# Kernel tuning notes

Hardware: AMD Instinct MI355X
Metric: run time of the kernel (lower is better)

The kernel has to match this reference:

```python
import jax, jax.numpy as jnp
import numpy as np

B, L, V = 64, 256, 8000
D_EMB = 100
D_MODEL = 256
H, DK = 4, 64
HID, HID2 = 256, 128   # bidirectional LSTM: 128 per direction
NT = 20                # tag_size
START, STOP = 18, 19


def setup_inputs() -> dict:
    key = jax.random.key(0)
    ks = jax.random.split(key, 32)
    s = 0.05
    inp = {}
    # forward args
    inp["sentences"] = jax.random.randint(ks[0], (B, L), 0, V)
    inp["bushou"] = jax.random.randint(ks[1], (B, L), 0, V)
    inp["pinyin"] = jax.random.normal(ks[2], (B, L, 20), dtype=jnp.float32)
    inp["weizhi"] = jax.random.normal(ks[3], (B, L, 18), dtype=jnp.float32)
    inp["trans_weizhi"] = jax.random.normal(ks[4], (B, L, 18), dtype=jnp.float32)
    inp["tags"] = jax.random.randint(ks[5], (B, L), 0, NT - 2)  # valid non-START/STOP tags
    inp["lengths"] = jax.random.randint(ks[6], (B,), L // 2, L + 1)
    # parameters
    inp["emb1"] = jax.random.normal(ks[7], (V, D_EMB)) * s
    inp["emb2"] = jax.random.normal(ks[8], (V, D_EMB)) * s
    inp["Wq"] = jax.random.normal(ks[9], (D_MODEL, D_MODEL)) * s
    inp["bq"] = jnp.zeros((D_MODEL,))
    inp["Wk"] = jax.random.normal(ks[10], (D_MODEL, D_MODEL)) * s
    inp["bk"] = jnp.zeros((D_MODEL,))
    inp["Wv"] = jax.random.normal(ks[11], (D_MODEL, D_MODEL)) * s
    inp["bv"] = jnp.zeros((D_MODEL,))
    inp["Wo"] = jax.random.normal(ks[12], (D_MODEL, D_MODEL)) * s
    inp["bo"] = jnp.zeros((D_MODEL,))
    # LSTM (torch layout): W_ih [4*HID2, D_MODEL], W_hh [4*HID2, HID2]; gate order i,f,g,o
    inp["Wih_f"] = jax.random.normal(ks[13], (4 * HID2, D_MODEL)) * s
    inp["Whh_f"] = jax.random.normal(ks[14], (4 * HID2, HID2)) * s
    inp["bih_f"] = jnp.zeros((4 * HID2,))
    inp["bhh_f"] = jnp.zeros((4 * HID2,))
    inp["Wih_b"] = jax.random.normal(ks[15], (4 * HID2, D_MODEL)) * s
    inp["Whh_b"] = jax.random.normal(ks[16], (4 * HID2, HID2)) * s
    inp["bih_b"] = jnp.zeros((4 * HID2,))
    inp["bhh_b"] = jnp.zeros((4 * HID2,))
    inp["Wout"] = jax.random.normal(ks[17], (NT, HID)) * s
    inp["bout"] = jnp.zeros((NT,))
    trans = jax.random.normal(ks[18], (NT, NT))
    trans = trans.at[:, START].set(-1000.0)
    trans = trans.at[STOP, :].set(-1000.0)
    inp["transitions"] = trans
    inp["h0"] = jax.random.normal(ks[19], (2, B, HID2))
    inp["c0"] = jax.random.normal(ks[20], (2, B, HID2))
    return inp


def _lstm_dir(x_tbd, Wih, Whh, bih, bhh, h0, c0, reverse):
    def step(carry, xt):
        h, c = carry
        g = xt @ Wih.T + bih + h @ Whh.T + bhh
        i, f, gg, o = jnp.split(g, 4, axis=-1)
        c = jax.nn.sigmoid(f) * c + jax.nn.sigmoid(i) * jnp.tanh(gg)
        h = jax.nn.sigmoid(o) * jnp.tanh(c)
        return (h, c), h
    _, ys = jax.lax.scan(step, (h0, c0), x_tbd, reverse=reverse)
    return ys  # [L, B, HID2], time-aligned


def reference(sentences, bushou, pinyin, weizhi, trans_weizhi, tags, lengths,
              emb1, emb2, Wq, bq, Wk, bk, Wv, bv, Wo, bo,
              Wih_f, Whh_f, bih_f, bhh_f, Wih_b, Whh_b, bih_b, bhh_b,
              Wout, bout, transitions, h0, c0):
    # feature concat: [emb1, emb2, pinyin, trans_weizhi, weizhi] -> [B,L,256]
    fin = jnp.concatenate([emb1[sentences], emb2[bushou], pinyin, trans_weizhi, weizhi], axis=2)

    def proj(W, b):
        return (fin @ W.T + b).reshape(B, L, H, DK).transpose(0, 2, 1, 3)  # [B,H,L,DK]
    q, k, v = proj(Wq, bq), proj(Wk, bk), proj(Wv, bv)
    scores = jnp.einsum('bhqd,bhkd->bhqk', q, k) / np.sqrt(DK).astype(np.float32)
    p = jax.nn.softmax(scores, axis=-1)  # dropout = identity at eval
    x = jnp.einsum('bhqk,bhkd->bhqd', p, v).transpose(0, 2, 1, 3).reshape(B, L, D_MODEL)
    x = x @ Wo.T + bo

    x_tbd = x.transpose(1, 0, 2)  # [L,B,256]
    out_f = _lstm_dir(x_tbd, Wih_f, Whh_f, bih_f, bhh_f, h0[0], c0[0], False)
    out_b = _lstm_dir(x_tbd, Wih_b, Whh_b, bih_b, bhh_b, h0[1], c0[1], True)
    lstm_out = jnp.concatenate([out_f, out_b], axis=-1).transpose(1, 0, 2)  # [B,L,256]
    logits = lstm_out @ Wout.T + bout  # [B,L,NT]

    mask = (jnp.arange(L)[None, :] < lengths[:, None])  # [B,L] valid positions

    # real path score (vectorized over batch, masked to length)
    lab = jnp.concatenate([jnp.full((B, 1), START, dtype=tags.dtype), tags], axis=1)  # [B,L+1]
    emis = jnp.take_along_axis(logits, tags[..., None], axis=2)[..., 0]  # [B,L]
    trans_step = transitions[lab[:, :-1], lab[:, 1:]]  # [B,L]
    last_tag = jnp.take_along_axis(tags, (lengths - 1)[:, None], axis=1)[:, 0]
    real = jnp.sum((emis + trans_step) * mask, axis=1) + transitions[last_tag, STOP]  # [B]

    # CRF forward algorithm (original initializes previous = zeros)
    def fstep(prev, inputs):
        logit_t, m_t = inputs  # [B,NT], [B]
        sc = prev[:, :, None] + transitions[None, :, :] + logit_t[:, None, :]  # [B,NT_prev,NT_cur]
        new = jax.nn.logsumexp(sc, axis=1)
        return jnp.where(m_t[:, None], new, prev), None
    prev0 = jnp.zeros((B, NT), dtype=logits.dtype)
    prev, _ = jax.lax.scan(fstep, prev0, (logits.transpose(1, 0, 2), mask.T))
    total = jax.nn.logsumexp(prev + transitions[:, STOP][None, :], axis=1)  # [B]

    return jnp.sum(total - real)  # neg log likelihood, summed over batch
```

## Files before the change

kernel.cpp:

```cpp
#include <hip/hip_runtime.h>
#include <math.h>

namespace {
constexpr int Bc = 64, Lc = 256, DMc = 256;
constexpr int NTc = 20, START_c = 18, STOP_c = 19;
constexpr int ROWSc = Bc * Lc;
}

typedef short short8 __attribute__((ext_vector_type(8)));
typedef float f32x4 __attribute__((ext_vector_type(4)));
typedef ushort ushort4v __attribute__((ext_vector_type(4)));
typedef unsigned int uint4v __attribute__((ext_vector_type(4)));

__device__ __forceinline__ ushort f2bf(float x) {
  unsigned u = __float_as_uint(x);
  unsigned r = (u + 0x7FFFu + ((u >> 16) & 1u)) >> 16;
  return (ushort)r;
}
__device__ __forceinline__ float bf2f(ushort h) {
  return __uint_as_float((unsigned)h << 16);
}
__device__ __forceinline__ float vrcp(float x) {
  float r;
  asm("v_rcp_f32 %0, %1" : "=v"(r) : "v"(x));
  return r;
}
__device__ __forceinline__ float fast_sig(float x) {
  return vrcp(1.f + __expf(-x));
}
__device__ __forceinline__ float fast_tanh(float x) {
  return fmaf(-2.f, vrcp(1.f + __expf(2.f * x)), 1.f);
}
__device__ __forceinline__ unsigned cvtpk(float a, float b) {
  unsigned r;
  asm("v_cvt_pk_bf16_f32 %0, %1, %2" : "=v"(r) : "v"(a), "v"(b));
  return r;
}

__global__ __launch_bounds__(256) void build_fin_k(
    const int* __restrict__ sent, const int* __restrict__ bush,
    const float* __restrict__ pin, const float* __restrict__ wz,
    const float* __restrict__ twz, const float* __restrict__ emb1,
    const float* __restrict__ emb2, ushort* __restrict__ finb) {
  const int row = blockIdx.x;
  const int c = threadIdx.x;
  float v;
  if (c < 100)      v = emb1[(size_t)sent[row] * 100 + c];
  else if (c < 200) v = emb2[(size_t)bush[row] * 100 + (c - 100)];
  else if (c < 220) v = pin[(size_t)row * 20 + (c - 200)];
  else if (c < 238) v = twz[(size_t)row * 18 + (c - 220)];
  else              v = wz[(size_t)row * 18 + (c - 238)];
  finb[(size_t)row * 256 + c] = f2bf(v);
}

__global__ __launch_bounds__(256) void prep_k(
    const float* __restrict__ Wq, const float* __restrict__ Wk,
    const float* __restrict__ Wv, const float* __restrict__ Wo,
    const float* __restrict__ Wihf, const float* __restrict__ Wihb,
    const float* __restrict__ Whhf, const float* __restrict__ Whhb,
    const float* __restrict__ Wout,
    const float* __restrict__ bq, const float* __restrict__ bk,
    const float* __restrict__ bv, const float* __restrict__ bo,
    const float* __restrict__ bihf, const float* __restrict__ bihb,
    ushort* __restrict__ wqkv, ushort* __restrict__ wih,
    ushort* __restrict__ whh, float* __restrict__ woutp,
    ushort* __restrict__ woT, float* __restrict__ bqkv,
    float* __restrict__ bcomb, float* __restrict__ zbias) {
  const int blk = blockIdx.x;
  const int tid = threadIdx.x;
  if (blk < 224) {
    const int gid = blk * 256 + tid;
    const int row = gid >> 5;
    if (row < 1792) {
      const int cl = (gid & 31) * 8;
      const float* src;
      ushort* dst;
      if (row < 768) {
        src = (row < 256 ? Wq : (row < 512 ? Wk : Wv)) + (size_t)(row & 255) * 256;
        dst = wqkv + (size_t)row * 256;
      } else {
        const int rr = row - 768;
        src = (rr < 512 ? Wihf + (size_t)rr * 256 : Wihb + (size_t)(rr - 512) * 256);
        dst = wih + (size_t)rr * 256;
      }
      float4 v0 = *(const float4*)(src + cl);
      float4 v1 = *(const float4*)(src + cl + 4);
      short8 o;
      o[0] = (short)f2bf(v0.x); o[1] = (short)f2bf(v0.y); o[2] = (short)f2bf(v0.z); o[3] = (short)f2bf(v0.w);
      o[4] = (short)f2bf(v1.x); o[5] = (short)f2bf(v1.y); o[6] = (short)f2bf(v1.z); o[7] = (short)f2bf(v1.w);
      *(short8*)(dst + cl) = o;
      if (gid < 768) {
        bqkv[gid] = (gid < 256 ? bq[gid] : (gid < 512 ? bk[gid - 256] : bv[gid - 512]));
      }
    }
  } else if (blk < 288) {
    const int gid = (blk - 224) * 256 + tid;
    const int idx = gid * 8;
    const float* src = (idx < 65536) ? (Whhf + idx) : (Whhb + (idx - 65536));
    float4 v0 = *(const float4*)(src);
    float4 v1 = *(const float4*)(src + 4);
    short8 o;
    o[0] = (short)f2bf(v0.x); o[1] = (short)f2bf(v0.y); o[2] = (short)f2bf(v0.z); o[3] = (short)f2bf(v0.w);
    o[4] = (short)f2bf(v1.x); o[5] = (short)f2bf(v1.y); o[6] = (short)f2bf(v1.z); o[7] = (short)f2bf(v1.w);
    *(short8*)(whh + idx) = o;
  } else if (blk < 308) {
    const int o = (blk - 288) * 256 + tid;
    const int n = o >> 8, rest = o & 255;
    const int pc = rest >> 2, uu = rest & 3;
    const int dir = pc >> 5, w = (pc >> 2) & 7, kg = pc & 3;
    woutp[o] = Wout[n * 256 + dir * 128 + w * 16 + kg * 4 + uu];
  } else if (blk < 564) {
    const int o = (blk - 308) * 256 + tid;
    const int k = o >> 8, n = o & 255;
    woT[o] = f2bf(Wo[n * 256 + k]);
  } else if (blk < 568) {
    const int j = (blk - 564) * 256 + tid;
    const float* wr = (j < 512) ? (Wihf + (size_t)j * 256) : (Wihb + (size_t)(j - 512) * 256);
    float s = (j < 512) ? bihf[j] : bihb[j - 512];
    for (int k = 0; k < 256; k += 4) {
      float4 w4 = *(const float4*)(wr + k);
      float4 b4 = *(const float4*)(bo + k);
      s += w4.x * b4.x + w4.y * b4.y + w4.z * b4.z + w4.w * b4.w;
    }
    bcomb[j] = s;
  } else {
    zbias[tid] = 0.f;
  }
}

template <int N, bool BF16_OUT>
__global__ __launch_bounds__(256, 2) void mfma_gemm_k(
    const ushort* __restrict__ A, const ushort* __restrict__ W,
    const float* __restrict__ bias, void* __restrict__ Cv) {
  __shared__ __align__(16) ushort As[128 * 256];
  const int tid = threadIdx.x, lane = tid & 63, wid = tid >> 6;
  const int bm = blockIdx.x * 128, bn = blockIdx.y * 128;
  const int wm = (wid >> 1) * 64, wn = (wid & 1) * 64;
  const int r = lane & 15, kg = lane >> 4;
#pragma unroll
  for (int i = 0; i < 16; ++i) {
    const int c = i * 256 + tid;
    const int row = c >> 5, kc = c & 31;
    short8 v = *(const short8*)(A + (size_t)(bm + row) * 256 + kc * 8);
    *(short8*)((char*)As + row * 512 + ((kc * 16) ^ ((row & 7) << 4))) = v;
  }
  const ushort* Wp = W + (size_t)(bn + wn + r) * 256 + kg * 8;
  f32x4 acc[4][4];
#pragma unroll
  for (int i = 0; i < 4; ++i)
#pragma unroll
    for (int j = 0; j < 4; ++j) acc[i][j] = (f32x4){0.f, 0.f, 0.f, 0.f};
  __syncthreads();
#pragma unroll
  for (int k0 = 0; k0 < 256; k0 += 32) {
    short8 a[4], b[4];
#pragma unroll
    for (int fi = 0; fi < 4; ++fi) {
      const int row = wm + fi * 16 + r;
      a[fi] = *(const short8*)((const char*)As + row * 512 +
                               ((k0 * 2 + kg * 16) ^ ((row & 7) << 4)));
    }
#pragma unroll
    for (int fj = 0; fj < 4; ++fj) b[fj] = *(const short8*)(Wp + fj * 16 * 256 + k0);
#pragma unroll
    for (int fi = 0; fi < 4; ++fi)
#pragma unroll
      for (int fj = 0; fj < 4; ++fj)
        acc[fi][fj] = __builtin_amdgcn_mfma_f32_16x16x32_bf16(a[fi], b[fj], acc[fi][fj], 0, 0, 0);
  }
#pragma unroll
  for (int fi = 0; fi < 4; ++fi)
#pragma unroll
    for (int fj = 0; fj < 4; ++fj) {
      const int n = bn + wn + fj * 16 + r;
      const float bn_ = bias[n];
#pragma unroll
      for (int rr = 0; rr < 4; ++rr) {
        const int m = bm + wm + fi * 16 + kg * 4 + rr;
        const float v = acc[fi][fj][rr] + bn_;
        if (BF16_OUT) ((ushort*)Cv)[(size_t)m * N + n] = f2bf(v);
        else          ((float*)Cv)[(size_t)m * N + n] = v;
      }
    }
}

__global__ __launch_bounds__(256) void attn_mfma_k(
    const ushort* __restrict__ qkv, ushort* __restrict__ xout) {
  extern __shared__ ushort smem[];
  ushort* Klds = smem;
  ushort* Vlds = smem + 16384;
  const int bh = blockIdx.x;
  const int b = bh >> 2, h = bh & 3;
  const int tid = threadIdx.x;
  const int lane = tid & 63, w = tid >> 6;
  const int r = lane & 15, kg = lane >> 4;
  const ushort* qb = qkv + (size_t)(b * Lc) * 768 + h * 64;
  const ushort* kb = qb + 256;
  const ushort* vb = qb + 512;
#pragma unroll
  for (int i = 0; i < 8; ++i) {
    const int c = i * 256 + tid;
    const int key = c >> 3, kc = c & 7;
    short8 v = *(const short8*)(kb + (size_t)key * 768 + kc * 8);
    *(short8*)((char*)Klds + key * 128 + ((kc * 16) ^ ((key & 7) << 4))) = v;
  }
#pragma unroll
  for (int i = 0; i < 8; ++i) {
    const int c = i * 256 + tid;
    const int key = c >> 3, dc = c & 7;
    short8 v = *(const short8*)(vb + (size_t)key * 768 + dc * 8);
#pragma unroll
    for (int j = 0; j < 8; ++j) {
      const int d = dc * 8 + j;
      *(ushort*)((char*)Vlds + d * 512 + ((key * 2) ^ ((d & 7) << 4))) = (ushort)v[j];
    }
  }
  __syncthreads();

#pragma unroll 1
  for (int it = 0; it < 4; ++it) {
    const int qbase = it * 64 + w * 16;
    short8 bq0 = *(const short8*)(qb + (size_t)(qbase + r) * 768 + kg * 8);
    short8 bq1 = *(const short8*)(qb + (size_t)(qbase + r) * 768 + 32 + kg * 8);
    f32x4 accs[16];
#pragma unroll
    for (int fi = 0; fi < 16; ++fi) accs[fi] = (f32x4){0.f, 0.f, 0.f, 0.f};
#pragma unroll
    for (int fi = 0; fi < 16; ++fi) {
      const int key = fi * 16 + r;
      short8 ak0 = *(const short8*)((const char*)Klds + key * 128 + ((kg * 16) ^ ((key & 7) << 4)));
      short8 ak1 = *(const short8*)((const char*)Klds + key * 128 + ((64 + kg * 16) ^ ((key & 7) << 4)));
      accs[fi] = __builtin_amdgcn_mfma_f32_16x16x32_bf16(ak0, bq0, accs[fi], 0, 0, 0);
      accs[fi] = __builtin_amdgcn_mfma_f32_16x16x32_bf16(ak1, bq1, accs[fi], 0, 0, 0);
    }
    float m = -1e30f;
#pragma unroll
    for (int fi = 0; fi < 16; ++fi)
#pragma unroll
      for (int rr = 0; rr < 4; ++rr) m = fmaxf(m, accs[fi][rr]);
    m = fmaxf(m, __shfl_xor(m, 16));
    m = fmaxf(m, __shfl_xor(m, 32));
    float den = 0.f;
#pragma unroll
    for (int fi = 0; fi < 16; ++fi)
#pragma unroll
      for (int rr = 0; rr < 4; ++rr) {
        const float e = __expf((accs[fi][rr] - m) * 0.125f);
        accs[fi][rr] = e;
        den += e;
      }
    den += __shfl_xor(den, 16);
    den += __shfl_xor(den, 32);
    const float rp = vrcp(den);
    unsigned u[16][2];
#pragma unroll
    for (int fi = 0; fi < 16; ++fi) {
      u[fi][0] = cvtpk(accs[fi][0] * rp, accs[fi][1] * rp);
      u[fi][1] = cvtpk(accs[fi][2] * rp, accs[fi][3] * rp);
    }
    short8 bpv[8];
#pragma unroll
    for (int ks2 = 0; ks2 < 8; ++ks2) {
      uint4v vals;
#pragma unroll
      for (int m2 = 0; m2 < 4; ++m2) {
        const int src = r + (((kg & 1) * 2 + (m2 >> 1)) << 4);
        const unsigned lo = __shfl(u[2 * ks2][m2 & 1], src);
        const unsigned hi = __shfl(u[2 * ks2 + 1][m2 & 1], src);
        vals[m2] = (kg >= 2) ? hi : lo;
      }
      union { uint4v u4; short8 s8; } cv;
      cv.u4 = vals;
      bpv[ks2] = cv.s8;
    }
    f32x4 acco[4];
#pragma unroll
    for (int fj = 0; fj < 4; ++fj) acco[fj] = (f32x4){0.f, 0.f, 0.f, 0.f};
#pragma unroll
    for (int fj = 0; fj < 4; ++fj) {
      const int d = fj * 16 + r;
#pragma unroll
      for (int ks2 = 0; ks2 < 8; ++ks2) {
        short8 bv = *(const short8*)((const char*)Vlds + d * 512 +
                                     ((ks2 * 64 + kg * 16) ^ ((d & 7) << 4)));
        acco[fj] = __builtin_amdgcn_mfma_f32_16x16x32_bf16(bpv[ks2], bv, acco[fj], 0, 0, 0);
      }
    }
#pragma unroll
    for (int fj = 0; fj < 4; ++fj)
#pragma unroll
      for (int rr = 0; rr < 4; ++rr) {
        const int q = qbase + kg * 4 + rr;
        xout[((size_t)(b * Lc + q)) * 256 + h * 64 + fj * 16 + r] = f2bf(acco[fj][rr]);
      }
  }
}

__global__ __launch_bounds__(256) void transpose_gx_k(
    const ushort* __restrict__ gx, const float* __restrict__ bhhf,
    const float* __restrict__ bhhb, ushort* __restrict__ gxt) {
  const int s = blockIdx.x, dir = blockIdx.y;
  const int t = threadIdx.x;
  const int b = t & 63;
  const int c = t >> 6;
  const float* bhh = dir ? bhhb : bhhf;
  const size_t obase = (size_t)(s * 2 + dir) * 32768;
#pragma unroll 4
  for (int i = 0; i < 16; ++i) {
    const int g8 = i * 4 + c;
    short8 v = *(const short8*)(gx + ((size_t)b * 256 + s) * 1024 + dir * 512 + g8 * 8);
    float f[8];
#pragma unroll
    for (int j = 0; j < 8; ++j) f[j] = bf2f((ushort)v[j]) + bhh[g8 * 8 + j];
    uint2 lo = make_uint2(cvtpk(f[0], f[1]), cvtpk(f[2], f[3]));
    uint2 hi = make_uint2(cvtpk(f[4], f[5]), cvtpk(f[6], f[7]));
    *(uint2*)(gxt + obase + (size_t)(g8 * 2) * 256 + b * 4) = lo;
    *(uint2*)(gxt + obase + (size_t)(g8 * 2 + 1) * 256 + b * 4) = hi;
  }
}

__global__ __launch_bounds__(512, 2) void lstm_mfma_k(
    const ushort* __restrict__ gxt, const ushort* __restrict__ whh,
    const float* __restrict__ h0, const float* __restrict__ c0,
    ushort* __restrict__ louts) {
  const int bs = blockIdx.x * 16;
  const int dir = blockIdx.y;
  const int tid = threadIdx.x;
  const int w = tid >> 6, lane = tid & 63;
  const int col = lane & 15;
  const int kg = lane >> 4;
  short8 afrag[4][4];
#pragma unroll
  for (int g = 0; g < 4; ++g)
#pragma unroll
    for (int ks = 0; ks < 4; ++ks)
      afrag[g][ks] = *(const short8*)(whh + (size_t)dir * 65536 +
                                      (size_t)(g * 128 + w * 16 + col) * 128 + ks * 32 + kg * 8);
  float4 c4 = *(const float4*)(c0 + (size_t)(dir * Bc + bs + col) * 128 + w * 16 + kg * 4);
  __shared__ __align__(16) ushort hlds[2][2048];
  {
    float4 h4 = *(const float4*)(h0 + (size_t)(dir * Bc + bs + col) * 128 + w * 16 + kg * 4);
    const int wb = (col * 256 + w * 32 + kg * 8) ^ ((col & 7) << 4);
    *(uint2*)((char*)hlds[0] + wb) = make_uint2(cvtpk(h4.x, h4.y), cvtpk(h4.z, h4.w));
  }
  const ushort* gtb = gxt + (size_t)dir * 32768 + (size_t)(w * 4 + kg) * 256 + (size_t)(bs + col) * 4;
  int step = dir ? (Lc - 1) : 0;
  const int dstep = dir ? -1 : 1;
  ushort4v gA[4], gB[4];
#pragma unroll
  for (int g = 0; g < 4; ++g) gA[g] = *(const ushort4v*)(gtb + (size_t)step * 65536 + g * 8192);
#pragma unroll
  for (int g = 0; g < 4; ++g) gB[g] = *(const ushort4v*)(gtb + (size_t)(step + dstep) * 65536 + g * 8192);
  __syncthreads();
  int p = 0;

  auto body = [&](ushort4v (&gcur)[4], int pfstep, bool pfok) {
    short8 bfrag[4];
#pragma unroll
    for (int ks = 0; ks < 4; ++ks) {
      const int rb = (col * 256 + ks * 64 + kg * 16) ^ ((col & 7) << 4);
      bfrag[ks] = *(const short8*)((const char*)hlds[p] + rb);
    }
    f32x4 acc[4];
#pragma unroll
    for (int g = 0; g < 4; ++g)
      acc[g] = (f32x4){bf2f(gcur[g][0]), bf2f(gcur[g][1]), bf2f(gcur[g][2]), bf2f(gcur[g][3])};
    if (pfok) {
#pragma unroll
      for (int g = 0; g < 4; ++g) gcur[g] = *(const ushort4v*)(gtb + (size_t)pfstep * 65536 + g * 8192);
    }
#pragma unroll
    for (int ks = 0; ks < 4; ++ks)
#pragma unroll
      for (int g = 0; g < 4; ++g)
        acc[g] = __builtin_amdgcn_mfma_f32_16x16x32_bf16(afrag[g][ks], bfrag[ks], acc[g], 0, 0, 0);
    f32x4 hr;
#pragma unroll
    for (int r = 0; r < 4; ++r) {
      const float ii = fast_sig (acc[0][r]);
      const float ff = fast_sig (acc[1][r]);
      const float gg = fast_tanh(acc[2][r]);
      const float oo = fast_sig (acc[3][r]);
      const float cn = ff * c4[r] + ii * gg;
      c4[r] = cn;
      hr[r] = oo * fast_tanh(cn);
    }
    const uint2 hp2 = make_uint2(cvtpk(hr[0], hr[1]), cvtpk(hr[2], hr[3]));
    const int wb = (col * 256 + w * 32 + kg * 8) ^ ((col & 7) << 4);
    *(uint2*)((char*)hlds[p ^ 1] + wb) = hp2;
    *(uint2*)(louts + (size_t)step * 16384 + dir * 8192 + w * 1024 + kg * 256 +
              (size_t)(bs + col) * 4) = hp2;
    asm volatile("s_waitcnt lgkmcnt(0)" ::: "memory");
    __builtin_amdgcn_s_barrier();
    asm volatile("" ::: "memory");
    p ^= 1;
    step += dstep;
  };

  for (int s = 0; s < Lc; s += 2) {
    const int pf1 = step + 2 * dstep;
    body(gA, pf1, s + 2 < Lc);
    const int pf2 = step + 2 * dstep;
    body(gB, pf2, s + 3 < Lc);
  }
}

__global__ __launch_bounds__(256) void logits_k(
    const ushort* __restrict__ louts, const float* __restrict__ woutp,
    const float* __restrict__ bout, float* __restrict__ lg) {
  const int s = blockIdx.x;
  const int t = threadIdx.x;
  __shared__ __align__(16) ushort xs[16384];
  __shared__ float wls[20 * 256];
  __shared__ float bls[20];
  {
    const ushort* src = louts + (size_t)s * 16384;
#pragma unroll
    for (int i = 0; i < 8; ++i)
      *(short8*)(xs + i * 2048 + t * 8) = *(const short8*)(src + i * 2048 + t * 8);
    for (int i = t; i < 20 * 256; i += 256) wls[i] = woutp[i];
    if (t < 20) bls[t] = bout[t];
  }
  __syncthreads();
  const int b = t & 63, tg = t >> 6;
  float acc[5] = {0.f, 0.f, 0.f, 0.f, 0.f};
  for (int pc = 0; pc < 64; ++pc) {
    ushort4v x4 = *(const ushort4v*)(xs + pc * 256 + b * 4);
    const float x0 = bf2f(x4[0]), x1 = bf2f(x4[1]), x2 = bf2f(x4[2]), x3 = bf2f(x4[3]);
#pragma unroll
    for (int n = 0; n < 5; ++n) {
      const float* w4 = wls + (tg * 5 + n) * 256 + pc * 4;
      acc[n] += x0 * w4[0] + x1 * w4[1] + x2 * w4[2] + x3 * w4[3];
    }
  }
#pragma unroll
  for (int n = 0; n < 5; ++n)
    lg[((size_t)b * Lc + s) * NTc + tg * 5 + n] = acc[n] + bls[tg * 5 + n];
}

__global__ __launch_bounds__(64) void crf_fwd_k(
    const float* __restrict__ lg, const int* __restrict__ tags,
    const int* __restrict__ lens, const float* __restrict__ tr,
    float* __restrict__ part) {
  const int b = blockIdx.x, j = threadIdx.x;
  __shared__ float tl[NTc * NTc];
  for (int i = j; i < NTc * NTc; i += 64) tl[i] = tr[i];
  __syncthreads();
  const int len = lens[b];
  float gv = 0.f;
  for (int t = j; t < len; t += 64) {
    const int tag = tags[b * Lc + t];
    const int pv = (t == 0) ? START_c : tags[b * Lc + t - 1];
    gv += lg[((size_t)b * Lc + t) * NTc + tag] + tl[pv * NTc + tag];
  }
#pragma unroll
  for (int off = 32; off > 0; off >>= 1) gv += __shfl_xor(gv, off);
  float trc[NTc];
#pragma unroll
  for (int i = 0; i < NTc; ++i) trc[i] = tl[i * NTc + ((j < NTc) ? j : 0)];
  float prevj = 0.f;
  float lgn = lg[(size_t)b * Lc * NTc + ((j < NTc) ? j : 0)];
  for (int t = 0; t < len; ++t) {
    const float lgc = lgn;
    if (t + 1 < len) lgn = lg[((size_t)b * Lc + t + 1) * NTc + ((j < NTc) ? j : 0)];
    float v[NTc];
    float m = -1e30f;
#pragma unroll
    for (int i = 0; i < NTc; ++i) {
      v[i] = __shfl(prevj, i) + trc[i];
      m = fmaxf(m, v[i]);
    }
    float ssum = 0.f;
#pragma unroll
    for (int i = 0; i < NTc; ++i) ssum += __expf(v[i] - m);
    prevj = m + __logf(ssum) + lgc;
  }
  float fv[NTc];
  float m = -1e30f;
#pragma unroll
  for (int i = 0; i < NTc; ++i) {
    fv[i] = __shfl(prevj, i) + tl[i * NTc + STOP_c];
    m = fmaxf(m, fv[i]);
  }
  float ssum = 0.f;
#pragma unroll
  for (int i = 0; i < NTc; ++i) ssum += __expf(fv[i] - m);
  if (j == 0) {
    const int lt = tags[b * Lc + len - 1];
    const float realv = gv + tl[lt * NTc + STOP_c];
    part[b] = (m + __logf(ssum)) - realv;
  }
}

__global__ __launch_bounds__(64) void final_sum_k(const float* __restrict__ part, float* __restrict__ out) {
  float v = part[threadIdx.x];
#pragma unroll
  for (int off = 32; off > 0; off >>= 1) v += __shfl_down(v, off);
  if (threadIdx.x == 0) out[0] = v;
}

extern "C" void kernel_launch(void* const* d_in, const int* in_sizes, int n_in,
                              void* d_out, int out_size, void* d_ws, size_t ws_size,
                              hipStream_t stream) {
  const int* sent = (const int*)d_in[0];
  const int* bush = (const int*)d_in[1];
  const float* pin = (const float*)d_in[2];
  const float* wz = (const float*)d_in[3];
  const float* twz = (const float*)d_in[4];
  const int* tags = (const int*)d_in[5];
  const int* lens = (const int*)d_in[6];
  const float* emb1 = (const float*)d_in[7];
  const float* emb2 = (const float*)d_in[8];
  const float* Wq = (const float*)d_in[9];  const float* bq = (const float*)d_in[10];
  const float* Wk = (const float*)d_in[11]; const float* bk = (const float*)d_in[12];
  const float* Wv = (const float*)d_in[13]; const float* bv = (const float*)d_in[14];
  const float* Wo = (const float*)d_in[15]; const float* bo = (const float*)d_in[16];
  const float* Wihf = (const float*)d_in[17]; const float* Whhf = (const float*)d_in[18];
  const float* bihf = (const float*)d_in[19]; const float* bhhf = (const float*)d_in[20];
  const float* Wihb = (const float*)d_in[21]; const float* Whhb = (const float*)d_in[22];
  const float* bihb = (const float*)d_in[23]; const float* bhhb = (const float*)d_in[24];
  const float* Wout = (const float*)d_in[25]; const float* bout = (const float*)d_in[26];
  const float* trans = (const float*)d_in[27];
  const float* h0 = (const float*)d_in[28]; const float* c0 = (const float*)d_in[29];
  float* out = (float*)d_out;
  float* w = (float*)d_ws;
  ushort* finb  = (ushort*)w;
  ushort* axb   = (ushort*)w;
  ushort* qkvb  = (ushort*)(w + 2097152);
  ushort* gxb   = (ushort*)(w + 8388608);
  ushort* gxt   = (ushort*)w;
  ushort* louts = (ushort*)(w + 8388608);
  float*  lgts  = w + 10485760;
  size_t off = 16777216;
  ushort* wqkvb  = (ushort*)(w + off); off += 768 * 256 / 2;
  ushort* wihbf  = (ushort*)(w + off); off += 1024 * 256 / 2;
  ushort* woTb   = (ushort*)(w + off); off += 256 * 256 / 2;
  ushort* wcombb = (ushort*)(w + off); off += 1024 * 256 / 2;
  ushort* whhp   = (ushort*)(w + off); off += 2 * 512 * 128 / 2;
  float* woutp = w + off; off += 20 * 256;
  float* bqkv  = w + off; off += 768;
  float* bcomb = w + off; off += 1024;
  float* zbias = w + off; off += 256;
  float* partv = w + off;

  prep_k<<<569, 256, 0, stream>>>(Wq, Wk, Wv, Wo, Wihf, Wihb, Whhf, Whhb, Wout,
                                  bq, bk, bv, bo, bihf, bihb,
                                  wqkvb, wihbf, whhp, woutp, woTb, bqkv, bcomb, zbias);
  build_fin_k<<<ROWSc, 256, 0, stream>>>(sent, bush, pin, wz, twz, emb1, emb2, finb);
  mfma_gemm_k<256, true><<<dim3(8, 2), 256, 0, stream>>>(wihbf, woTb, zbias, wcombb);
  mfma_gemm_k<768, true><<<dim3(128, 6), 256, 0, stream>>>(finb, wqkvb, bqkv, qkvb);
  attn_mfma_k<<<Bc * 4, 256, 65536, stream>>>(qkvb, axb);
  mfma_gemm_k<1024, true><<<dim3(128, 8), 256, 0, stream>>>(axb, wcombb, bcomb, gxb);
  transpose_gx_k<<<dim3(256, 2), 256, 0, stream>>>(gxb, bhhf, bhhb, gxt);
  lstm_mfma_k<<<dim3(4, 2), 512, 0, stream>>>(gxt, whhp, h0, c0, louts);
  logits_k<<<Lc, 256, 0, stream>>>(louts, woutp, bout, lgts);
  crf_fwd_k<<<Bc, 64, 0, stream>>>(lgts, tags, lens, trans, partv);
  final_sum_k<<<1, 64, 0, stream>>>(partv, out);
}
```

Before: 493.5 us.

## Fold log2e scaling into LSTM weights, merge prep kernels, streamline CRF and logits

The prep and embedding-build kernels are merged into one launch. W_hh and the input-gate preactivations are pre-scaled by -log2(e), so the LSTM gates use raw v_exp_f32 and pointer increments replace per-step index math. The CRF forward switches to base-2 exp/log with a tree max and split sums, and the logits kernel reads LSTM outputs straight from global memory instead of staging them in LDS. These changes cut launch overhead and per-step instruction count on the serial LSTM and CRF paths. The cost is bf16 rounding of pre-scaled values, which can shift numerics slightly.

```diff
diff --git a/kernel.cpp b/kernel.cpp
--- a/kernel.cpp
+++ b/kernel.cpp
@@ -5,6 +5,7 @@
 constexpr int Bc = 64, Lc = 256, DMc = 256;
 constexpr int NTc = 20, START_c = 18, STOP_c = 19;
 constexpr int ROWSc = Bc * Lc;
+constexpr float NL2E = -1.4426950408889634f;
 }
 
 typedef short short8 __attribute__((ext_vector_type(8)));
@@ -25,11 +26,18 @@
   asm("v_rcp_f32 %0, %1" : "=v"(r) : "v"(x));
   return r;
 }
+__device__ __forceinline__ float vexp2(float x) {
+  float r;
+  asm("v_exp_f32 %0, %1" : "=v"(r) : "v"(x));
+  return r;
+}
+__device__ __forceinline__ float vlog2(float x) {
+  float r;
+  asm("v_log_f32 %0, %1" : "=v"(r) : "v"(x));
+  return r;
+}
 __device__ __forceinline__ float fast_sig(float x) {
   return vrcp(1.f + __expf(-x));
-}
-__device__ __forceinline__ float fast_tanh(float x) {
-  return fmaf(-2.f, vrcp(1.f + __expf(2.f * x)), 1.f);
 }
 __device__ __forceinline__ unsigned cvtpk(float a, float b) {
   unsigned r;
@@ -37,23 +45,11 @@
   return r;
 }
 
-__global__ __launch_bounds__(256) void build_fin_k(
+__global__ __launch_bounds__(256) void prep_fin_k(
     const int* __restrict__ sent, const int* __restrict__ bush,
     const float* __restrict__ pin, const float* __restrict__ wz,
     const float* __restrict__ twz, const float* __restrict__ emb1,
-    const float* __restrict__ emb2, ushort* __restrict__ finb) {
-  const int row = blockIdx.x;
-  const int c = threadIdx.x;
-  float v;
-  if (c < 100)      v = emb1[(size_t)sent[row] * 100 + c];
-  else if (c < 200) v = emb2[(size_t)bush[row] * 100 + (c - 100)];
-  else if (c < 220) v = pin[(size_t)row * 20 + (c - 200)];
-  else if (c < 238) v = twz[(size_t)row * 18 + (c - 220)];
-  else              v = wz[(size_t)row * 18 + (c - 238)];
-  finb[(size_t)row * 256 + c] = f2bf(v);
-}
-
-__global__ __launch_bounds__(256) void prep_k(
+    const float* __restrict__ emb2, ushort* __restrict__ finb,
     const float* __restrict__ Wq, const float* __restrict__ Wk,
     const float* __restrict__ Wv, const float* __restrict__ Wo,
     const float* __restrict__ Wihf, const float* __restrict__ Wihb,
@@ -66,8 +62,20 @@
     ushort* __restrict__ whh, float* __restrict__ woutp,
     ushort* __restrict__ woT, float* __restrict__ bqkv,
     float* __restrict__ bcomb, float* __restrict__ zbias) {
-  const int blk = blockIdx.x;
   const int tid = threadIdx.x;
+  if (blockIdx.x < 16384) {
+    const int row = blockIdx.x;
+    const int c = tid;
+    float v;
+    if (c < 100)      v = emb1[(size_t)sent[row] * 100 + c];
+    else if (c < 200) v = emb2[(size_t)bush[row] * 100 + (c - 100)];
+    else if (c < 220) v = pin[(size_t)row * 20 + (c - 200)];
+    else if (c < 238) v = twz[(size_t)row * 18 + (c - 220)];
+    else              v = wz[(size_t)row * 18 + (c - 238)];
+    finb[(size_t)row * 256 + c] = f2bf(v);
+    return;
+  }
+  const int blk = blockIdx.x - 16384;
   if (blk < 224) {
     const int gid = blk * 256 + tid;
     const int row = gid >> 5;
@@ -100,8 +108,10 @@
     float4 v0 = *(const float4*)(src);
     float4 v1 = *(const float4*)(src + 4);
     short8 o;
-    o[0] = (short)f2bf(v0.x); o[1] = (short)f2bf(v0.y); o[2] = (short)f2bf(v0.z); o[3] = (short)f2bf(v0.w);
-    o[4] = (short)f2bf(v1.x); o[5] = (short)f2bf(v1.y); o[6] = (short)f2bf(v1.z); o[7] = (short)f2bf(v1.w);
+    o[0] = (short)f2bf(v0.x * NL2E); o[1] = (short)f2bf(v0.y * NL2E);
+    o[2] = (short)f2bf(v0.z * NL2E); o[3] = (short)f2bf(v0.w * NL2E);
+    o[4] = (short)f2bf(v1.x * NL2E); o[5] = (short)f2bf(v1.y * NL2E);
+    o[6] = (short)f2bf(v1.z * NL2E); o[7] = (short)f2bf(v1.w * NL2E);
     *(short8*)(whh + idx) = o;
   } else if (blk < 308) {
     const int o = (blk - 288) * 256 + tid;
@@ -311,7 +321,7 @@
     short8 v = *(const short8*)(gx + ((size_t)b * 256 + s) * 1024 + dir * 512 + g8 * 8);
     float f[8];
 #pragma unroll
-    for (int j = 0; j < 8; ++j) f[j] = bf2f((ushort)v[j]) + bhh[g8 * 8 + j];
+    for (int j = 0; j < 8; ++j) f[j] = (bf2f((ushort)v[j]) + bhh[g8 * 8 + j]) * NL2E;
     uint2 lo = make_uint2(cvtpk(f[0], f[1]), cvtpk(f[2], f[3]));
     uint2 hi = make_uint2(cvtpk(f[4], f[5]), cvtpk(f[6], f[7]));
     *(uint2*)(gxt + obase + (size_t)(g8 * 2) * 256 + b * 4) = lo;
@@ -344,17 +354,22 @@
     *(uint2*)((char*)hlds[0] + wb) = make_uint2(cvtpk(h4.x, h4.y), cvtpk(h4.z, h4.w));
   }
   const ushort* gtb = gxt + (size_t)dir * 32768 + (size_t)(w * 4 + kg) * 256 + (size_t)(bs + col) * 4;
-  int step = dir ? (Lc - 1) : 0;
+  const int step0 = dir ? (Lc - 1) : 0;
   const int dstep = dir ? -1 : 1;
+  const ptrdiff_t gstride = (ptrdiff_t)dstep * 65536;
+  const ptrdiff_t lstride = (ptrdiff_t)dstep * 16384;
   ushort4v gA[4], gB[4];
 #pragma unroll
-  for (int g = 0; g < 4; ++g) gA[g] = *(const ushort4v*)(gtb + (size_t)step * 65536 + g * 8192);
-#pragma unroll
-  for (int g = 0; g < 4; ++g) gB[g] = *(const ushort4v*)(gtb + (size_t)(step + dstep) * 65536 + g * 8192);
+  for (int g = 0; g < 4; ++g) gA[g] = *(const ushort4v*)(gtb + (size_t)step0 * 65536 + g * 8192);
+#pragma unroll
+  for (int g = 0; g < 4; ++g) gB[g] = *(const ushort4v*)(gtb + (size_t)(step0 + dstep) * 65536 + g * 8192);
+  const ushort* gld = gtb + (size_t)step0 * 65536 + 2 * gstride;
+  ushort* lst = louts + (size_t)step0 * 16384 + dir * 8192 + w * 1024 + kg * 256 +
+                (size_t)(bs + col) * 4;
   __syncthreads();
   int p = 0;
 
-  auto body = [&](ushort4v (&gcur)[4], int pfstep, bool pfok) {
+  auto body = [&](ushort4v (&gcur)[4], bool pfok) {
     short8 bfrag[4];
 #pragma unroll
     for (int ks = 0; ks < 4; ++ks) {
@@ -367,7 +382,8 @@
       acc[g] = (f32x4){bf2f(gcur[g][0]), bf2f(gcur[g][1]), bf2f(gcur[g][2]), bf2f(gcur[g][3])};
     if (pfok) {
 #pragma unroll
-      for (int g = 0; g < 4; ++g) gcur[g] = *(const ushort4v*)(gtb + (size_t)pfstep * 65536 + g * 8192);
+      for (int g = 0; g < 4; ++g) gcur[g] = *(const ushort4v*)(gld + g * 8192);
+      gld += gstride;
     }
 #pragma unroll
     for (int ks = 0; ks < 4; ++ks)
@@ -377,31 +393,29 @@
     f32x4 hr;
 #pragma unroll
     for (int r = 0; r < 4; ++r) {
-      const float ii = fast_sig (acc[0][r]);
-      const float ff = fast_sig (acc[1][r]);
-      const float gg = fast_tanh(acc[2][r]);
-      const float oo = fast_sig (acc[3][r]);
+      const float ii = vrcp(1.f + vexp2(acc[0][r]));
+      const float ff = vrcp(1.f + vexp2(acc[1][r]));
+      const float gg = fmaf(-2.f, vrcp(1.f + vexp2(acc[2][r] * -2.f)), 1.f);
+      const float oo = vrcp(1.f + vexp2(acc[3][r]));
       const float cn = ff * c4[r] + ii * gg;
       c4[r] = cn;
-      hr[r] = oo * fast_tanh(cn);
+      const float tc = fmaf(-2.f, vrcp(1.f + vexp2(cn * 2.8853900817779268f)), 1.f);
+      hr[r] = oo * tc;
     }
     const uint2 hp2 = make_uint2(cvtpk(hr[0], hr[1]), cvtpk(hr[2], hr[3]));
     const int wb = (col * 256 + w * 32 + kg * 8) ^ ((col & 7) << 4);
     *(uint2*)((char*)hlds[p ^ 1] + wb) = hp2;
-    *(uint2*)(louts + (size_t)step * 16384 + dir * 8192 + w * 1024 + kg * 256 +
-              (size_t)(bs + col) * 4) = hp2;
+    *(uint2*)lst = hp2;
+    lst += lstride;
     asm volatile("s_waitcnt lgkmcnt(0)" ::: "memory");
     __builtin_amdgcn_s_barrier();
     asm volatile("" ::: "memory");
     p ^= 1;
-    step += dstep;
   };
 
   for (int s = 0; s < Lc; s += 2) {
-    const int pf1 = step + 2 * dstep;
-    body(gA, pf1, s + 2 < Lc);
-    const int pf2 = step + 2 * dstep;
-    body(gB, pf2, s + 3 < Lc);
+    body(gA, s + 2 < Lc);
+    body(gB, s + 3 < Lc);
   }
 }
 
@@ -410,22 +424,16 @@
     const float* __restrict__ bout, float* __restrict__ lg) {
   const int s = blockIdx.x;
   const int t = threadIdx.x;
-  __shared__ __align__(16) ushort xs[16384];
   __shared__ float wls[20 * 256];
   __shared__ float bls[20];
-  {
-    const ushort* src = louts + (size_t)s * 16384;
-#pragma unroll
-    for (int i = 0; i < 8; ++i)
-      *(short8*)(xs + i * 2048 + t * 8) = *(const short8*)(src + i * 2048 + t * 8);
-    for (int i = t; i < 20 * 256; i += 256) wls[i] = woutp[i];
-    if (t < 20) bls[t] = bout[t];
-  }
+  for (int i = t; i < 20 * 256; i += 256) wls[i] = woutp[i];
+  if (t < 20) bls[t] = bout[t];
   __syncthreads();
   const int b = t & 63, tg = t >> 6;
+  const ushort* src = louts + (size_t)s * 16384 + b * 4;
   float acc[5] = {0.f, 0.f, 0.f, 0.f, 0.f};
   for (int pc = 0; pc < 64; ++pc) {
-    ushort4v x4 = *(const ushort4v*)(xs + pc * 256 + b * 4);
+    ushort4v x4 = *(const ushort4v*)(src + pc * 256);
     const float x0 = bf2f(x4[0]), x1 = bf2f(x4[1]), x2 = bf2f(x4[2]), x3 = bf2f(x4[3]);
 #pragma unroll
     for (int n = 0; n < 5; ++n) {
@@ -443,6 +451,7 @@
     const int* __restrict__ lens, const float* __restrict__ tr,
     float* __restrict__ part) {
   const int b = blockIdx.x, j = threadIdx.x;
+  const float L2E = 1.4426950408889634f;
   __shared__ float tl[NTc * NTc];
   for (int i = j; i < NTc * NTc; i += 64) tl[i] = tr[i];
   __syncthreads();
@@ -455,40 +464,53 @@
   }
 #pragma unroll
   for (int off = 32; off > 0; off >>= 1) gv += __shfl_xor(gv, off);
-  float trc[NTc];
-#pragma unroll
-  for (int i = 0; i < NTc; ++i) trc[i] = tl[i * NTc + ((j < NTc) ? j : 0)];
-  float prevj = 0.f;
-  float lgn = lg[(size_t)b * Lc * NTc + ((j < NTc) ? j : 0)];
+  const int jj = (j < NTc) ? j : 0;
+  float trc2[NTc];
+#pragma unroll
+  for (int i = 0; i < NTc; ++i) trc2[i] = tl[i * NTc + jj] * L2E;
+  float prev2 = 0.f;
+  float lgn = lg[(size_t)b * Lc * NTc + jj];
   for (int t = 0; t < len; ++t) {
-    const float lgc = lgn;
-    if (t + 1 < len) lgn = lg[((size_t)b * Lc + t + 1) * NTc + ((j < NTc) ? j : 0)];
+    const float lg2 = lgn * L2E;
+    if (t + 1 < len) lgn = lg[((size_t)b * Lc + t + 1) * NTc + jj];
     float v[NTc];
-    float m = -1e30f;
-#pragma unroll
-    for (int i = 0; i < NTc; ++i) {
-      v[i] = __shfl(prevj, i) + trc[i];
-      m = fmaxf(m, v[i]);
-    }
-    float ssum = 0.f;
-#pragma unroll
-    for (int i = 0; i < NTc; ++i) ssum += __expf(v[i] - m);
-    prevj = m + __logf(ssum) + lgc;
+#pragma unroll
+    for (int i = 0; i < NTc; ++i) v[i] = __shfl(prev2, i) + trc2[i];
+    float a0 = fmaxf(v[0], v[1]), a1 = fmaxf(v[2], v[3]), a2 = fmaxf(v[4], v[5]);
+    float a3 = fmaxf(v[6], v[7]), a4 = fmaxf(v[8], v[9]), a5 = fmaxf(v[10], v[11]);
+    float a6 = fmaxf(v[12], v[13]), a7 = fmaxf(v[14], v[15]), a8 = fmaxf(v[16], v[17]);
+    float a9 = fmaxf(v[18], v[19]);
+    float b0 = fmaxf(fmaxf(a0, a1), a2), b1 = fmaxf(fmaxf(a3, a4), a5);
+    float b2 = fmaxf(fmaxf(a6, a7), a8);
+    const float m = fmaxf(fmaxf(b0, b1), fmaxf(b2, a9));
+    float s0 = 0.f, s1 = 0.f, s2 = 0.f, s3 = 0.f;
+#pragma unroll
+    for (int i = 0; i < NTc; i += 4) {
+      s0 += vexp2(v[i] - m);
+      s1 += vexp2(v[i + 1] - m);
+      s2 += vexp2(v[i + 2] - m);
+      s3 += vexp2(v[i + 3] - m);
+    }
+    prev2 = m + vlog2((s0 + s1) + (s2 + s3)) + lg2;
   }
   float fv[NTc];
-  float m = -1e30f;
-#pragma unroll
-  for (int i = 0; i < NTc; ++i) {
-    fv[i] = __shfl(prevj, i) + tl[i * NTc + STOP_c];
-    m = fmaxf(m, fv[i]);
-  }
+#pragma unroll
+  for (int i = 0; i < NTc; ++i) fv[i] = __shfl(prev2, i) + tl[i * NTc + STOP_c] * L2E;
+  float a0 = fmaxf(fv[0], fv[1]), a1 = fmaxf(fv[2], fv[3]), a2 = fmaxf(fv[4], fv[5]);
+  float a3 = fmaxf(fv[6], fv[7]), a4 = fmaxf(fv[8], fv[9]), a5 = fmaxf(fv[10], fv[11]);
+  float a6 = fmaxf(fv[12], fv[13]), a7 = fmaxf(fv[14], fv[15]), a8 = fmaxf(fv[16], fv[17]);
+  float a9 = fmaxf(fv[18], fv[19]);
+  float b0 = fmaxf(fmaxf(a0, a1), a2), b1 = fmaxf(fmaxf(a3, a4), a5);
+  float b2 = fmaxf(fmaxf(a6, a7), a8);
+  const float m = fmaxf(fmaxf(b0, b1), fmaxf(b2, a9));
   float ssum = 0.f;
 #pragma unroll
-  for (int i = 0; i < NTc; ++i) ssum += __expf(fv[i] - m);
+  for (int i = 0; i < NTc; ++i) ssum += vexp2(fv[i] - m);
   if (j == 0) {
     const int lt = tags[b * Lc + len - 1];
     const float realv = gv + tl[lt * NTc + STOP_c];
-    part[b] = (m + __logf(ssum)) - realv;
+    const float total = (m + vlog2(ssum)) * 0.6931471805599453f;
+    part[b] = total - realv;
   }
 }
 
@@ -543,10 +565,11 @@
   float* zbias = w + off; off += 256;
   float* partv = w + off;
 
-  prep_k<<<569, 256, 0, stream>>>(Wq, Wk, Wv, Wo, Wihf, Wihb, Whhf, Whhb, Wout,
-                                  bq, bk, bv, bo, bihf, bihb,
-                                  wqkvb, wihbf, whhp, woutp, woTb, bqkv, bcomb, zbias);
-  build_fin_k<<<ROWSc, 256, 0, stream>>>(sent, bush, pin, wz, twz, emb1, emb2, finb);
+  prep_fin_k<<<16384 + 569, 256, 0, stream>>>(
+      sent, bush, pin, wz, twz, emb1, emb2, finb,
+      Wq, Wk, Wv, Wo, Wihf, Wihb, Whhf, Whhb, Wout,
+      bq, bk, bv, bo, bihf, bihb,
+      wqkvb, wihbf, whhp, woutp, woTb, bqkv, bcomb, zbias);
   mfma_gemm_k<256, true><<<dim3(8, 2), 256, 0, stream>>>(wihbf, woTb, zbias, wcombb);
   mfma_gemm_k<768, true><<<dim3(128, 6), 256, 0, stream>>>(finb, wqkvb, bqkv, qkvb);
   attn_mfma_k<<<Bc * 4, 256, 65536, stream>>>(qkvb, axb);
```

Result: faster. 463.8 us (-6.0%).
